# Performance work log

Measured on AMD Instinct MI355X. Metric: run time of the kernel, lower is better.

The kernel has to match this reference:

```python
import jax, jax.numpy as jnp
import numpy as np

F = 256   # num_features
H = 64    # num_hidden_features
B = 8192  # batch


def setup_inputs() -> dict:
    key = jax.random.key(0)
    ks = jax.random.split(key, 7)
    s1 = 1.0  # torch Linear init scale ~ U(-1/sqrt(fan_in), ...); use normal*1/sqrt(fan_in)
    sH = 1.0 / np.sqrt(H)
    x = jax.random.normal(ks[0], (B, F), dtype=jnp.float32)
    # Stacked per-feature weights. torch Linear: y = x @ W.T + b, W:[out,in].
    w1 = jax.random.normal(ks[1], (F, H), dtype=jnp.float32) * s1      # [F, H]  (in=1)
    b1 = jax.random.normal(ks[2], (F, H), dtype=jnp.float32) * s1
    w2 = jax.random.normal(ks[3], (F, H, H), dtype=jnp.float32) * sH   # [F, out, in]
    b2 = jax.random.normal(ks[4], (F, H), dtype=jnp.float32) * sH
    w3 = jax.random.normal(ks[5], (F, H), dtype=jnp.float32) * sH      # [F, H] (out=1)
    b3 = jax.random.normal(ks[6], (F,), dtype=jnp.float32) * sH
    return {"x": x, "w1": w1, "b1": b1, "w2": w2, "b2": b2, "w3": w3, "b3": b3}


def reference(x, w1, b1, w2, b2, w3, b3):
    # x: [B, F]; per-feature MLP 1 -> H -> H -> 1, fused via batched einsums.
    h1 = jax.nn.relu(x[:, :, None] * w1[None, :, :] + b1[None])        # [B, F, H]
    h2 = jax.nn.relu(jnp.einsum('bfh,foh->bfo', h1, w2) + b2[None])    # [B, F, H]
    out = jnp.einsum('bfh,fh->bf', h2, w3) + b3[None]                  # [B, F]
    return out
```

## Files before the change

kernel.cpp:

```cpp
#include <hip/hip_runtime.h>
#include <hip/hip_bf16.h>


namespace {

constexpr int kF = 256;
constexpr int kH = 64;
constexpr int kB = 8192;

constexpr int kFPB     = 4;
constexpr int kRPB     = 128;
constexpr int kThreads = 256;
constexpr int kFG      = kF / kFPB;
constexpr int kRG      = kB / kRPB;
constexpr int kBlocks  = kFG * kRG;
constexpr int kPasses  = kRPB / 16;
constexpr int kXP      = 10;

using f32x2  = __attribute__((ext_vector_type(2))) float;
using f32x4  = __attribute__((ext_vector_type(4))) float;
using bf16x4 = __attribute__((ext_vector_type(4))) __bf16;
using bf16x8 = __attribute__((ext_vector_type(8))) __bf16;

__global__ __launch_bounds__(256)
void pack_params(const float* __restrict__ w2, const float* __restrict__ b2,
                 const float* __restrict__ w3, __bf16* __restrict__ w2p,
                 float* __restrict__ b2p, __bf16* __restrict__ w3p)
{
  const int wid  = (int)threadIdx.x >> 6;
  const int lane = (int)threadIdx.x & 63;
  const int f    = (int)blockIdx.x * 4 + wid;
  const int l15  = lane & 15;
  const int lg   = lane >> 4;

  const float* w2f = w2 + (size_t)f * (kH * kH);
  #pragma unroll
  for (int t = 0; t < 4; ++t) {
    const int o2 = 32 * (t >> 1) + 8 * (l15 >> 2) + 4 * (t & 1) + (l15 & 3);
    #pragma unroll
    for (int ks = 0; ks < 2; ++ks) {
      const float* p = w2f + o2 * kH + ks * 32 + lg * 8;
      const f32x4 lo = *reinterpret_cast<const f32x4*>(p);
      const f32x4 hi = *reinterpret_cast<const f32x4*>(p + 4);
      const bf16x8 v = __builtin_shufflevector(
          __builtin_convertvector(lo, bf16x4),
          __builtin_convertvector(hi, bf16x4), 0, 1, 2, 3, 4, 5, 6, 7);
      *reinterpret_cast<bf16x8*>(
          w2p + (((size_t)f * 8 + t * 2 + ks) * 64 + lane) * 8) = v;
    }
  }

  {
    const int jt = lane >> 4, jlg = (lane >> 2) & 3, jr = lane & 3;
    const int o  = 32 * (jt >> 1) + 8 * jlg + 4 * (jt & 1) + jr;
    b2p[(size_t)f * kH + lane] = b2[(size_t)f * kH + o];
  }
  w3p[(size_t)f * kH + lane] = (__bf16)w3[(size_t)f * kH + lane];
}

__global__ __launch_bounds__(kThreads, 3)
void mlp_pf_v11(const float* __restrict__ x,
                const float* __restrict__ w1,
                const float* __restrict__ b1,
                const __bf16* __restrict__ w2p,
                const float* __restrict__ b2p,
                const __bf16* __restrict__ w3p,
                const float* __restrict__ b3,
                float* __restrict__ out)
{
  __shared__ float xs[kFPB][16][kXP];
  __shared__ float outb[kRPB][kFPB + 1];

  const int tid  = (int)threadIdx.x;
  const int wid  = tid >> 6;
  const int lane = tid & 63;
  const int l15  = lane & 15;
  const int lg   = lane >> 4;

  const int fg = (int)blockIdx.x & (kFG - 1);
  const int rg = (int)blockIdx.x >> 6;
  const int f  = fg * kFPB + wid;
  const int r0 = rg * kRPB;

  bf16x8 w2frag[4][2];
  {
    const __bf16* base = w2p + ((size_t)f * 8 * 64 + lane) * 8;
    #pragma unroll
    for (int t = 0; t < 4; ++t)
      #pragma unroll
      for (int ks = 0; ks < 2; ++ks)
        w2frag[t][ks] = *reinterpret_cast<const bf16x8*>(
            base + (size_t)(t * 2 + ks) * 64 * 8);
  }

  if (tid < kRPB) {
    const int rr = tid;
    const f32x4 v = *reinterpret_cast<const f32x4*>(
        x + (size_t)(r0 + rr) * kF + fg * kFPB);
    const int a = rr & 15, b = rr >> 4;
    xs[0][a][b] = v[0]; xs[1][a][b] = v[1];
    xs[2][a][b] = v[2]; xs[3][a][b] = v[3];
  }

  f32x4 w1v[2][2], b1v[2][2];
  #pragma unroll
  for (int ks = 0; ks < 2; ++ks) {
    const float* pw = w1 + f * kH + ks * 32 + lg * 8;
    const float* pb = b1 + f * kH + ks * 32 + lg * 8;
    w1v[ks][0] = *reinterpret_cast<const f32x4*>(pw);
    w1v[ks][1] = *reinterpret_cast<const f32x4*>(pw + 4);
    b1v[ks][0] = *reinterpret_cast<const f32x4*>(pb);
    b1v[ks][1] = *reinterpret_cast<const f32x4*>(pb + 4);
  }
  f32x4 b2c[4];
  #pragma unroll
  for (int t = 0; t < 4; ++t)
    b2c[t] = *reinterpret_cast<const f32x4*>(b2p + f * kH + t * 16 + lg * 4);
  bf16x8 w3f[2];
  #pragma unroll
  for (int ks = 0; ks < 2; ++ks)
    w3f[ks] = *reinterpret_cast<const bf16x8*>(w3p + f * kH + ks * 32 + lg * 8);
  const float b3v = b3[f];
  const f32x4 b3c = {b3v, b3v, b3v, b3v};

  __syncthreads();

  const f32x4 zero4 = {0.f, 0.f, 0.f, 0.f};
  float keep = 0.f;

  #pragma unroll
  for (int pp = 0; pp < kPasses / 2; ++pp) {
    const f32x2 xp = *reinterpret_cast<const f32x2*>(&xs[wid][l15][2 * pp]);

    bf16x8 h1A[2], h1B[2];
    #pragma unroll
    for (int ks = 0; ks < 2; ++ks) {
      f32x4 aA = w1v[ks][0] * xp[0] + b1v[ks][0];
      f32x4 bA = w1v[ks][1] * xp[0] + b1v[ks][1];
      f32x4 aB = w1v[ks][0] * xp[1] + b1v[ks][0];
      f32x4 bB = w1v[ks][1] * xp[1] + b1v[ks][1];
      aA = __builtin_elementwise_max(aA, zero4);
      bA = __builtin_elementwise_max(bA, zero4);
      aB = __builtin_elementwise_max(aB, zero4);
      bB = __builtin_elementwise_max(bB, zero4);
      h1A[ks] = __builtin_shufflevector(
          __builtin_convertvector(aA, bf16x4),
          __builtin_convertvector(bA, bf16x4), 0, 1, 2, 3, 4, 5, 6, 7);
      h1B[ks] = __builtin_shufflevector(
          __builtin_convertvector(aB, bf16x4),
          __builtin_convertvector(bB, bf16x4), 0, 1, 2, 3, 4, 5, 6, 7);
    }

    f32x4 accA[4], accB[4];
    #pragma unroll
    for (int t = 0; t < 4; ++t) {
      accA[t] = __builtin_amdgcn_mfma_f32_16x16x32_bf16(
          w2frag[t][0], h1A[0], b2c[t], 0, 0, 0);
      accB[t] = __builtin_amdgcn_mfma_f32_16x16x32_bf16(
          w2frag[t][0], h1B[0], b2c[t], 0, 0, 0);
      accA[t] = __builtin_amdgcn_mfma_f32_16x16x32_bf16(
          w2frag[t][1], h1A[1], accA[t], 0, 0, 0);
      accB[t] = __builtin_amdgcn_mfma_f32_16x16x32_bf16(
          w2frag[t][1], h1B[1], accB[t], 0, 0, 0);
    }

    bf16x8 h2A0, h2A1, h2B0, h2B1;
    {
      const f32x4 rA0 = __builtin_elementwise_max(accA[0], zero4);
      const f32x4 rA1 = __builtin_elementwise_max(accA[1], zero4);
      const f32x4 rA2 = __builtin_elementwise_max(accA[2], zero4);
      const f32x4 rA3 = __builtin_elementwise_max(accA[3], zero4);
      const f32x4 rB0 = __builtin_elementwise_max(accB[0], zero4);
      const f32x4 rB1 = __builtin_elementwise_max(accB[1], zero4);
      const f32x4 rB2 = __builtin_elementwise_max(accB[2], zero4);
      const f32x4 rB3 = __builtin_elementwise_max(accB[3], zero4);
      h2A0 = __builtin_shufflevector(__builtin_convertvector(rA0, bf16x4),
                                     __builtin_convertvector(rA1, bf16x4),
                                     0, 1, 2, 3, 4, 5, 6, 7);
      h2A1 = __builtin_shufflevector(__builtin_convertvector(rA2, bf16x4),
                                     __builtin_convertvector(rA3, bf16x4),
                                     0, 1, 2, 3, 4, 5, 6, 7);
      h2B0 = __builtin_shufflevector(__builtin_convertvector(rB0, bf16x4),
                                     __builtin_convertvector(rB1, bf16x4),
                                     0, 1, 2, 3, 4, 5, 6, 7);
      h2B1 = __builtin_shufflevector(__builtin_convertvector(rB2, bf16x4),
                                     __builtin_convertvector(rB3, bf16x4),
                                     0, 1, 2, 3, 4, 5, 6, 7);
    }

    f32x4 dA = __builtin_amdgcn_mfma_f32_16x16x32_bf16(w3f[0], h2A0, b3c, 0, 0, 0);
    f32x4 dB = __builtin_amdgcn_mfma_f32_16x16x32_bf16(w3f[0], h2B0, b3c, 0, 0, 0);
    dA = __builtin_amdgcn_mfma_f32_16x16x32_bf16(w3f[1], h2A1, dA, 0, 0, 0);
    dB = __builtin_amdgcn_mfma_f32_16x16x32_bf16(w3f[1], h2B1, dB, 0, 0, 0);

    const int pA = 2 * pp, pB = 2 * pp + 1;
    keep = (lg == (pA & 3)) ? dA[0] : keep;
    keep = (lg == (pB & 3)) ? dB[0] : keep;
    if ((pB & 3) == 3) {
      outb[(pB >> 2) * 64 + lane][wid] = keep;
    }
  }

  __syncthreads();

  if (tid < kRPB) {
    const int rr = tid;
    const f32x4 v = {outb[rr][0], outb[rr][1], outb[rr][2], outb[rr][3]};
    *reinterpret_cast<f32x4*>(out + (size_t)(r0 + rr) * kF + fg * kFPB) = v;
  }
}

}

extern "C" void kernel_launch(void* const* d_in, const int* in_sizes, int n_in,
                              void* d_out, int out_size, void* d_ws, size_t ws_size,
                              hipStream_t stream) {
  const float* x  = (const float*)d_in[0];
  const float* w1 = (const float*)d_in[1];
  const float* b1 = (const float*)d_in[2];
  const float* w2 = (const float*)d_in[3];
  const float* b2 = (const float*)d_in[4];
  const float* w3 = (const float*)d_in[5];
  const float* b3 = (const float*)d_in[6];
  float* out = (float*)d_out;

  __bf16* w2p = (__bf16*)d_ws;
  float*  b2p = (float*)((char*)d_ws + (2u << 20));
  __bf16* w3p = (__bf16*)((char*)d_ws + (2u << 20) + (64u << 10));

  hipLaunchKernelGGL(pack_params, dim3(kF / 4), dim3(256), 0, stream,
                     w2, b2, w3, w2p, b2p, w3p);
  hipLaunchKernelGGL(mlp_pf_v11, dim3(kBlocks), dim3(kThreads), 0, stream,
                     x, w1, b1, w2p, b2p, w3p, b3, out);
}
```

Measured before the change: 40.37 us.

## Compute first layer with MFMA using packed bf16 w1/b1 and x,1 operand

Moves the rank-1 first layer (x*w1+b1) from per-lane VALU FMAs onto MFMA instructions. w1 and b1 are packed as bf16 pairs in a prep kernel and multiplied against an [x, 1] bf16 vector, with all other K lanes zeroed. This offloads VALU work to the matrix units and reuses one pack helper for ReLU/convert. The cost is 8 extra MFMAs per pass and lower precision from rounding x, w1 and b1 to bf16.

New measurement: 42.50 us. 5.3% more time.

```diff
diff --git a/kernel.cpp b/kernel.cpp
--- a/kernel.cpp
+++ b/kernel.cpp
@@ -19,13 +19,16 @@
 
 using f32x2  = __attribute__((ext_vector_type(2))) float;
 using f32x4  = __attribute__((ext_vector_type(4))) float;
+using u32x4  = __attribute__((ext_vector_type(4))) unsigned;
 using bf16x4 = __attribute__((ext_vector_type(4))) __bf16;
 using bf16x8 = __attribute__((ext_vector_type(8))) __bf16;
 
 __global__ __launch_bounds__(256)
-void pack_params(const float* __restrict__ w2, const float* __restrict__ b2,
+void pack_params(const float* __restrict__ w1, const float* __restrict__ b1,
+                 const float* __restrict__ w2, const float* __restrict__ b2,
                  const float* __restrict__ w3, __bf16* __restrict__ w2p,
-                 float* __restrict__ b2p, __bf16* __restrict__ w3p)
+                 float* __restrict__ b2p, __bf16* __restrict__ w3p,
+                 unsigned* __restrict__ w1b1p)
 {
   const int wid  = (int)threadIdx.x >> 6;
   const int lane = (int)threadIdx.x & 63;
@@ -56,15 +59,25 @@
     b2p[(size_t)f * kH + lane] = b2[(size_t)f * kH + o];
   }
   w3p[(size_t)f * kH + lane] = (__bf16)w3[(size_t)f * kH + lane];
+
+  {
+    const int t = lane >> 4, m = lane & 15;
+    const int o1 = 32 * (t >> 1) + 8 * (m >> 2) + 4 * (t & 1) + (m & 3);
+    const __bf16 wv = (__bf16)w1[(size_t)f * kH + o1];
+    const __bf16 bv = (__bf16)b1[(size_t)f * kH + o1];
+    const unsigned u =
+        (unsigned)__builtin_bit_cast(unsigned short, wv) |
+        ((unsigned)__builtin_bit_cast(unsigned short, bv) << 16);
+    w1b1p[(size_t)f * 64 + lane] = u;
+  }
 }
 
 __global__ __launch_bounds__(kThreads, 3)
-void mlp_pf_v11(const float* __restrict__ x,
-                const float* __restrict__ w1,
-                const float* __restrict__ b1,
+void mlp_pf_v13(const float* __restrict__ x,
                 const __bf16* __restrict__ w2p,
                 const float* __restrict__ b2p,
                 const __bf16* __restrict__ w3p,
+                const unsigned* __restrict__ w1b1p,
                 const float* __restrict__ b3,
                 float* __restrict__ out)
 {
@@ -102,16 +115,18 @@
     xs[2][a][b] = v[2]; xs[3][a][b] = v[3];
   }
 
-  f32x4 w1v[2][2], b1v[2][2];
-  #pragma unroll
-  for (int ks = 0; ks < 2; ++ks) {
-    const float* pw = w1 + f * kH + ks * 32 + lg * 8;
-    const float* pb = b1 + f * kH + ks * 32 + lg * 8;
-    w1v[ks][0] = *reinterpret_cast<const f32x4*>(pw);
-    w1v[ks][1] = *reinterpret_cast<const f32x4*>(pw + 4);
-    b1v[ks][0] = *reinterpret_cast<const f32x4*>(pb);
-    b1v[ks][1] = *reinterpret_cast<const f32x4*>(pb + 4);
-  }
+  bf16x8 w1b1f[4];
+  {
+    const unsigned* wb = w1b1p + (size_t)f * 64;
+    #pragma unroll
+    for (int t = 0; t < 4; ++t) {
+      unsigned u = wb[t * 16 + l15];
+      u = (lg == 0) ? u : 0u;
+      const u32x4 q = {u, 0u, 0u, 0u};
+      w1b1f[t] = __builtin_bit_cast(bf16x8, q);
+    }
+  }
+
   f32x4 b2c[4];
   #pragma unroll
   for (int t = 0; t < 4; ++t)
@@ -128,65 +143,57 @@
   const f32x4 zero4 = {0.f, 0.f, 0.f, 0.f};
   float keep = 0.f;
 
+  auto make_xb = [&](float xvf) -> bf16x8 {
+    unsigned u =
+        (unsigned)__builtin_bit_cast(unsigned short, (__bf16)xvf) | 0x3F800000u;
+    u = (lg == 0) ? u : 0u;
+    const u32x4 q = {u, 0u, 0u, 0u};
+    return __builtin_bit_cast(bf16x8, q);
+  };
+  auto pack2 = [&](const f32x4& a, const f32x4& b) -> bf16x8 {
+    return __builtin_shufflevector(
+        __builtin_convertvector(__builtin_elementwise_max(a, zero4), bf16x4),
+        __builtin_convertvector(__builtin_elementwise_max(b, zero4), bf16x4),
+        0, 1, 2, 3, 4, 5, 6, 7);
+  };
+
   #pragma unroll
   for (int pp = 0; pp < kPasses / 2; ++pp) {
     const f32x2 xp = *reinterpret_cast<const f32x2*>(&xs[wid][l15][2 * pp]);
-
-    bf16x8 h1A[2], h1B[2];
-    #pragma unroll
-    for (int ks = 0; ks < 2; ++ks) {
-      f32x4 aA = w1v[ks][0] * xp[0] + b1v[ks][0];
-      f32x4 bA = w1v[ks][1] * xp[0] + b1v[ks][1];
-      f32x4 aB = w1v[ks][0] * xp[1] + b1v[ks][0];
-      f32x4 bB = w1v[ks][1] * xp[1] + b1v[ks][1];
-      aA = __builtin_elementwise_max(aA, zero4);
-      bA = __builtin_elementwise_max(bA, zero4);
-      aB = __builtin_elementwise_max(aB, zero4);
-      bB = __builtin_elementwise_max(bB, zero4);
-      h1A[ks] = __builtin_shufflevector(
-          __builtin_convertvector(aA, bf16x4),
-          __builtin_convertvector(bA, bf16x4), 0, 1, 2, 3, 4, 5, 6, 7);
-      h1B[ks] = __builtin_shufflevector(
-          __builtin_convertvector(aB, bf16x4),
-          __builtin_convertvector(bB, bf16x4), 0, 1, 2, 3, 4, 5, 6, 7);
-    }
+    const bf16x8 xbA = make_xb(xp[0]);
+    const bf16x8 xbB = make_xb(xp[1]);
+
+    f32x4 a1A[4], a1B[4];
+    #pragma unroll
+    for (int t = 0; t < 4; ++t) {
+      a1A[t] = __builtin_amdgcn_mfma_f32_16x16x32_bf16(
+          w1b1f[t], xbA, zero4, 0, 0, 0);
+      a1B[t] = __builtin_amdgcn_mfma_f32_16x16x32_bf16(
+          w1b1f[t], xbB, zero4, 0, 0, 0);
+    }
+
+    const bf16x8 h1A0 = pack2(a1A[0], a1A[1]);
+    const bf16x8 h1A1 = pack2(a1A[2], a1A[3]);
+    const bf16x8 h1B0 = pack2(a1B[0], a1B[1]);
+    const bf16x8 h1B1 = pack2(a1B[2], a1B[3]);
 
     f32x4 accA[4], accB[4];
     #pragma unroll
     for (int t = 0; t < 4; ++t) {
       accA[t] = __builtin_amdgcn_mfma_f32_16x16x32_bf16(
-          w2frag[t][0], h1A[0], b2c[t], 0, 0, 0);
+          w2frag[t][0], h1A0, b2c[t], 0, 0, 0);
       accB[t] = __builtin_amdgcn_mfma_f32_16x16x32_bf16(
-          w2frag[t][0], h1B[0], b2c[t], 0, 0, 0);
+          w2frag[t][0], h1B0, b2c[t], 0, 0, 0);
       accA[t] = __builtin_amdgcn_mfma_f32_16x16x32_bf16(
-          w2frag[t][1], h1A[1], accA[t], 0, 0, 0);
+          w2frag[t][1], h1A1, accA[t], 0, 0, 0);
       accB[t] = __builtin_amdgcn_mfma_f32_16x16x32_bf16(
-          w2frag[t][1], h1B[1], accB[t], 0, 0, 0);
-    }
-
-    bf16x8 h2A0, h2A1, h2B0, h2B1;
-    {
-      const f32x4 rA0 = __builtin_elementwise_max(accA[0], zero4);
-      const f32x4 rA1 = __builtin_elementwise_max(accA[1], zero4);
-      const f32x4 rA2 = __builtin_elementwise_max(accA[2], zero4);
-      const f32x4 rA3 = __builtin_elementwise_max(accA[3], zero4);
-      const f32x4 rB0 = __builtin_elementwise_max(accB[0], zero4);
-      const f32x4 rB1 = __builtin_elementwise_max(accB[1], zero4);
-      const f32x4 rB2 = __builtin_elementwise_max(accB[2], zero4);
-      const f32x4 rB3 = __builtin_elementwise_max(accB[3], zero4);
-      h2A0 = __builtin_shufflevector(__builtin_convertvector(rA0, bf16x4),
-                                     __builtin_convertvector(rA1, bf16x4),
-                                     0, 1, 2, 3, 4, 5, 6, 7);
-      h2A1 = __builtin_shufflevector(__builtin_convertvector(rA2, bf16x4),
-                                     __builtin_convertvector(rA3, bf16x4),
-                                     0, 1, 2, 3, 4, 5, 6, 7);
-      h2B0 = __builtin_shufflevector(__builtin_convertvector(rB0, bf16x4),
-                                     __builtin_convertvector(rB1, bf16x4),
-                                     0, 1, 2, 3, 4, 5, 6, 7);
-      h2B1 = __builtin_shufflevector(__builtin_convertvector(rB2, bf16x4),
-                                     __builtin_convertvector(rB3, bf16x4),
-                                     0, 1, 2, 3, 4, 5, 6, 7);
-    }
+          w2frag[t][1], h1B1, accB[t], 0, 0, 0);
+    }
+
+    const bf16x8 h2A0 = pack2(accA[0], accA[1]);
+    const bf16x8 h2A1 = pack2(accA[2], accA[3]);
+    const bf16x8 h2B0 = pack2(accB[0], accB[1]);
+    const bf16x8 h2B1 = pack2(accB[2], accB[3]);
 
     f32x4 dA = __builtin_amdgcn_mfma_f32_16x16x32_bf16(w3f[0], h2A0, b3c, 0, 0, 0);
     f32x4 dB = __builtin_amdgcn_mfma_f32_16x16x32_bf16(w3f[0], h2B0, b3c, 0, 0, 0);
@@ -224,12 +231,13 @@
   const float* b3 = (const float*)d_in[6];
   float* out = (float*)d_out;
 
-  __bf16* w2p = (__bf16*)d_ws;
-  float*  b2p = (float*)((char*)d_ws + (2u << 20));
-  __bf16* w3p = (__bf16*)((char*)d_ws + (2u << 20) + (64u << 10));
+  __bf16*   w2p   = (__bf16*)d_ws;
+  float*    b2p   = (float*)((char*)d_ws + (2u << 20));
+  __bf16*   w3p   = (__bf16*)((char*)d_ws + (2u << 20) + (64u << 10));
+  unsigned* w1b1p = (unsigned*)((char*)d_ws + (2u << 20) + (96u << 10));
 
   hipLaunchKernelGGL(pack_params, dim3(kF / 4), dim3(256), 0, stream,
-                     w2, b2, w3, w2p, b2p, w3p);
-  hipLaunchKernelGGL(mlp_pf_v11, dim3(kBlocks), dim3(kThreads), 0, stream,
-                     x, w1, b1, w2p, b2p, w3p, b3, out);
-}
+                     w1, b1, w2, b2, w3, w2p, b2p, w3p, w1b1p);
+  hipLaunchKernelGGL(mlp_pf_v13, dim3(kBlocks), dim3(kThreads), 0, stream,
+                     x, w2p, b2p, w3p, w1b1p, b3, out);
+}
```
